# Performance work log

Measured on AMD Instinct MI355X. Metric: run time of the kernel, lower is better.

The kernel has to match this reference:

```python
import jax, jax.numpy as jnp
import numpy as np

TOPK = 2


def setup_inputs() -> dict:
    key = jax.random.key(0)
    k1, k2 = jax.random.split(key)
    B, N, D, E, C = 4, 2048, 2048, 8, 512
    token_inputs = jax.random.normal(k1, (B, N, D), dtype=jnp.float32)
    # bottleneck_in.weight.t() stacked over experts: [E, D, C]; scaled like a real init
    bottleneck_weights = jax.random.normal(k2, (E, D, C), dtype=jnp.float32) * 0.02
    return {
        "token_inputs": token_inputs,
        "bottleneck_weights": bottleneck_weights,
        "expert_capacity": 640,
    }


def _routing(router_probs, expert_capacity, topk):
    # router_probs: [B, N, E]
    B, N, E = router_probs.shape
    _, expert_indices = jax.lax.top_k(router_probs, topk)      # [B, N, topk]
    idx = jnp.transpose(expert_indices, (0, 2, 1)).reshape(B, topk * N)
    expert_mask = jax.nn.one_hot(idx, E, dtype=jnp.int32)       # [B, topk*N, E]
    token_priority = jnp.cumsum(expert_mask, axis=1) * expert_mask - 1
    token_priority = token_priority.reshape(B, topk, N, E)
    token_priority = jnp.transpose(token_priority, (0, 2, 1, 3))  # [B, N, topk, E]
    token_priority = jnp.max(token_priority, axis=2)              # [B, N, E]
    # one-hot over capacity; negative (-1) and >= capacity priorities map to all-zero rows
    cap_range = jnp.arange(expert_capacity, dtype=jnp.int32)
    dispatch = (token_priority[..., None] == cap_range).astype(jnp.float32)  # [B,N,E,C]
    combine = router_probs[..., None] * dispatch                            # [B,N,E,C]
    return dispatch, combine


def reference(token_inputs, bottleneck_weights, expert_capacity):
    # activation_cache: [B, N, E, Cb]
    activation_cache = jnp.einsum("bnd,edc->bnec", token_inputs, bottleneck_weights)
    router_logits = jnp.sqrt(jnp.sum(activation_cache * activation_cache, axis=-1))  # [B,N,E]
    router_probs = jax.nn.softmax(router_logits, axis=-1)
    dispatch, combine = _routing(router_probs, expert_capacity, TOPK)
    return jnp.stack([dispatch, combine], axis=0)  # [2, B, N, E, capacity]
```

## Files before the change

kernel.cpp:

```cpp
#include <hip/hip_runtime.h>
#include <math.h>

constexpr int Bb = 4, Nn = 2048, Dd = 2048, Ee = 8, Cbn = 512;
constexpr int Mm = Bb * Nn;

typedef _Float16 half8 __attribute__((ext_vector_type(8)));
typedef float floatx16 __attribute__((ext_vector_type(16)));

#define GLL16(g, l)                                                     \
  __builtin_amdgcn_global_load_lds(                                     \
      (const __attribute__((address_space(1))) void*)(g),               \
      (__attribute__((address_space(3))) void*)(l), 16, 0, 0)

#define MFMA_F16(a, b, c) __builtin_amdgcn_mfma_f32_32x32x16_f16(a, b, c, 0, 0, 0)


__global__ __launch_bounds__(256) void transpose_w(const float* __restrict__ W,
                                                   _Float16* __restrict__ WT) {
  const int kt = blockIdx.x;
  const int ct = blockIdx.y;
  const int e = blockIdx.z;
  __shared__ _Float16 thi[64][72];
  __shared__ _Float16 tlo[64][72];
  const int tx = threadIdx.x & 15, ty = threadIdx.x >> 4;
  const float* src = W + ((size_t)(e * 2048 + kt * 64)) * 512 + ct * 64;
#pragma unroll
  for (int p = 0; p < 4; ++p) {
    int kk = ty + p * 16;
    float4 v = *(const float4*)(src + (size_t)kk * 512 + tx * 4);
    _Float16 hh;
    hh = (_Float16)v.x; thi[tx * 4 + 0][kk] = hh; tlo[tx * 4 + 0][kk] = (_Float16)(v.x - (float)hh);
    hh = (_Float16)v.y; thi[tx * 4 + 1][kk] = hh; tlo[tx * 4 + 1][kk] = (_Float16)(v.y - (float)hh);
    hh = (_Float16)v.z; thi[tx * 4 + 2][kk] = hh; tlo[tx * 4 + 2][kk] = (_Float16)(v.z - (float)hh);
    hh = (_Float16)v.w; thi[tx * 4 + 3][kk] = hh; tlo[tx * 4 + 3][kk] = (_Float16)(v.w - (float)hh);
  }
  __syncthreads();
  const int nt = e * 4 + (ct >> 1);
#pragma unroll
  for (int p = 0; p < 2; ++p) {
    int unit = threadIdx.x + p * 256;
    int ch = unit >> 6;
    int cc = unit & 63;
    int kt16 = kt * 4 + (ch >> 1);
    int chunk = ch & 1;
    int row = (ct & 1) * 64 + cc;
    _Float16* dst = WT + ((size_t)(nt * 128 + kt16)) * 4096 + chunk * 1024 + row * 8;
    *(half8*)dst = *(const half8*)(&thi[cc][ch * 8]);
    *(half8*)(dst + 2048) = *(const half8*)(&tlo[cc][ch * 8]);
  }
}

__global__ __launch_bounds__(256) void split_x(const float* __restrict__ X,
                                               _Float16* __restrict__ XT) {
  const int mt = blockIdx.x;
  const int kb = blockIdx.y;
  const int tid = threadIdx.x;
#pragma unroll
  for (int p = 0; p < 2; ++p) {
    const int u = tid + p * 256;
    const int c4 = u & 3;
    const int row = u >> 2;
    const float* src = X + ((size_t)(mt * 128 + row)) * 2048 + kb * 32 + c4 * 8;
    float4 a = *(const float4*)src;
    float4 b = *(const float4*)(src + 4);
    float f[8] = {a.x, a.y, a.z, a.w, b.x, b.y, b.z, b.w};
    half8 hi, lo;
#pragma unroll
    for (int j = 0; j < 8; ++j) {
      _Float16 hh = (_Float16)f[j];
      hi[j] = hh;
      lo[j] = (_Float16)(f[j] - (float)hh);
    }
    const int kt16 = kb * 2 + (c4 >> 1);
    const int chunk = c4 & 1;
    _Float16* dst = XT + ((size_t)(mt * 128 + kt16)) * 4096 + chunk * 1024 + row * 8;
    *(half8*)dst = hi;
    *(half8*)(dst + 2048) = lo;
  }
}

__global__ __launch_bounds__(512) void gemm_mfma(const _Float16* __restrict__ XT,
                                                 const _Float16* __restrict__ WT,
                                                 float* __restrict__ partial) {
  const int bid = blockIdx.x;
  const int swz = (bid & 7) * 64 + (bid >> 3);
  const int bM = swz >> 4;
  const int bN = swz & 15;

  const int tid = threadIdx.x;
  const int w = tid >> 6, l = tid & 63;
  const int wm = w >> 2, wn = w & 3;
  const int h = l >> 5, l31 = l & 31;

  __shared__ __align__(16) char lds[131072];

  const char* XTb = (const char*)XT;
  const char* WTb = (const char*)WT;
  const char* srcA[2];
  const char* srcB[2];
  int ldsAo[2], ldsBo[2];
#pragma unroll
  for (int q = 0; q < 2; ++q) {
    const int i3 = q * 4 + (w >> 1);
    srcA[q] = XTb + ((size_t)((bM * 2 + (i3 >> 2)) * 128)) * 8192 +
              (i3 & 3) * 2048 + (w & 1) * 1024 + l * 16;
    srcB[q] = WTb + ((size_t)((bN * 2 + (i3 >> 2)) * 128)) * 8192 +
              (i3 & 3) * 2048 + (w & 1) * 1024 + l * 16;
    ldsAo[q] = q * 8192 + w * 1024;
    ldsBo[q] = 16384 + q * 8192 + w * 1024;
  }

  int aoff[4][2], boff[2][2];
#pragma unroll
  for (int mf = 0; mf < 4; ++mf)
#pragma unroll
    for (int hl = 0; hl < 2; ++hl)
      aoff[mf][hl] = wm * 8192 + hl * 4096 + h * 2048 + (mf * 32 + l31) * 16;
#pragma unroll
  for (int nf = 0; nf < 2; ++nf)
#pragma unroll
    for (int hl = 0; hl < 2; ++hl)
      boff[nf][hl] = 16384 + (wn >> 1) * 8192 + hl * 4096 + h * 2048 +
                     ((wn & 1) * 64 + nf * 32 + l31) * 16;

  floatx16 acc[4][2] = {};

  auto stage = [&](int t) {
    const size_t ko = (size_t)t * 8192;
    char* base = lds + (t & 3) * 32768;
#pragma unroll
    for (int q = 0; q < 2; ++q) {
      GLL16(srcA[q] + ko, base + ldsAo[q]);
      GLL16(srcB[q] + ko, base + ldsBo[q]);
    }
  };
  auto compute = [&](int t) {
    const char* Lb = lds + (t & 3) * 32768;
    half8 ah[4], al[4], bh[2], bl[2];
#pragma unroll
    for (int mf = 0; mf < 4; ++mf) {
      ah[mf] = *(const half8*)(Lb + aoff[mf][0]);
      al[mf] = *(const half8*)(Lb + aoff[mf][1]);
    }
#pragma unroll
    for (int nf = 0; nf < 2; ++nf) {
      bh[nf] = *(const half8*)(Lb + boff[nf][0]);
      bl[nf] = *(const half8*)(Lb + boff[nf][1]);
    }
    __builtin_amdgcn_s_setprio(1);
#pragma unroll
    for (int mf = 0; mf < 4; ++mf)
#pragma unroll
      for (int nf = 0; nf < 2; ++nf) {
        acc[mf][nf] = MFMA_F16(ah[mf], bh[nf], acc[mf][nf]);
        acc[mf][nf] = MFMA_F16(ah[mf], bl[nf], acc[mf][nf]);
        acc[mf][nf] = MFMA_F16(al[mf], bh[nf], acc[mf][nf]);
      }
    __builtin_amdgcn_s_setprio(0);
  };

  stage(0);
  stage(1);
  stage(2);
  asm volatile("s_waitcnt vmcnt(8)" ::: "memory");
  __builtin_amdgcn_s_barrier();

  for (int kt = 0; kt < 125; ++kt) {
    stage(kt + 3);
    compute(kt);
    asm volatile("s_waitcnt vmcnt(8)" ::: "memory");
    __builtin_amdgcn_s_barrier();
  }
  asm volatile("s_waitcnt vmcnt(0)" ::: "memory");
  __builtin_amdgcn_s_barrier();
  compute(125);
  compute(126);
  compute(127);

  const int slice = bN * 4 + wn;
  float out0 = 0.f, out1 = 0.f;
#pragma unroll
  for (int j = 0; j < 2; ++j) {
    float mv = 0.f;
#pragma unroll
    for (int ii = 0; ii < 2; ++ii) {
      const floatx16& c0 = acc[j * 2 + ii][0];
      const floatx16& c1 = acc[j * 2 + ii][1];
#pragma unroll
      for (int reg = 0; reg < 16; ++reg) {
        float v = c0[reg] * c0[reg] + c1[reg] * c1[reg];
#pragma unroll
        for (int m = 1; m <= 16; m <<= 1) v += __shfl_xor(v, m, 64);
        if (l31 == ii * 16 + reg) mv = v;
      }
    }
    if (j == 0) out0 = mv; else out1 = mv;
  }
  {
    const int reg = l & 15;
    const int ii = l31 >> 4;
    const int rowin = (reg & 3) + 8 * (reg >> 2) + 4 * h;
    const int tok = bM * 256 + wm * 128 + ii * 32 + rowin;
    partial[(size_t)tok * 64 + slice] = out0;
    partial[(size_t)(tok + 64) * 64 + slice] = out1;
  }
}

__global__ void route_kernel(const float* __restrict__ partial,
                             int* __restrict__ idx1, int* __restrict__ idx2,
                             float* __restrict__ p1, float* __restrict__ p2) {
  int t = blockIdx.x * blockDim.x + threadIdx.x;
  if (t >= Mm) return;
  float l[Ee];
  float mx = -1e30f;
#pragma unroll
  for (int e = 0; e < Ee; ++e) {
    float s = 0.f;
#pragma unroll
    for (int u = 0; u < 8; ++u) s += partial[(size_t)t * 64 + e * 8 + u];
    l[e] = sqrtf(s);
    mx = fmaxf(mx, l[e]);
  }
  float p[Ee];
  float s = 0.f;
#pragma unroll
  for (int e = 0; e < Ee; ++e) {
    p[e] = expf(l[e] - mx);
    s += p[e];
  }
  float inv = 1.f / s;
  int i1 = 0;
  float b1 = l[0];
#pragma unroll
  for (int e = 1; e < Ee; ++e)
    if (l[e] > b1) { b1 = l[e]; i1 = e; }
  int i2 = -1;
  float b2 = -1e30f;
#pragma unroll
  for (int e = 0; e < Ee; ++e)
    if (e != i1 && l[e] > b2) { b2 = l[e]; i2 = e; }
  idx1[t] = i1;
  idx2[t] = i2;
  p1[t] = p[i1] * inv;
  p2[t] = p[i2] * inv;
}

__global__ void scan_kernel(const int* __restrict__ idx1,
                            const int* __restrict__ idx2,
                            int* __restrict__ prios) {
  const int b = blockIdx.x;
  const int tid = threadIdx.x;
  __shared__ int cnts[256][8];
  int cnt[8] = {0, 0, 0, 0, 0, 0, 0, 0};
  int eloc[16];
  const int base_p = tid * 16;
#pragma unroll
  for (int i = 0; i < 16; ++i) {
    int p = base_p + i;
    int k = p >> 11;
    int n = p & (Nn - 1);
    int e = (k == 0 ? idx1 : idx2)[b * Nn + n];
    eloc[i] = e;
    cnt[e]++;
  }
#pragma unroll
  for (int e = 0; e < 8; ++e) cnts[tid][e] = cnt[e];
  __syncthreads();
  if (tid < 8) {
    int run = 0;
    for (int i = 0; i < 256; ++i) {
      int v = cnts[i][tid];
      cnts[i][tid] = run;
      run += v;
    }
  }
  __syncthreads();
  int base[8];
#pragma unroll
  for (int e = 0; e < 8; ++e) base[e] = cnts[tid][e];
#pragma unroll
  for (int i = 0; i < 16; ++i) {
    int e = eloc[i];
    prios[b * 2 * Nn + base_p + i] = base[e]++;
  }
}

__global__ __launch_bounds__(256) void zscatter_kernel(const int* __restrict__ idx1,
                                                       const int* __restrict__ idx2,
                                                       const float* __restrict__ p1,
                                                       const float* __restrict__ p2,
                                                       const int* __restrict__ prios,
                                                       float* __restrict__ out, int cap) {
  const int t = blockIdx.x;
  const int ec = Ee * cap;
  float4* o1 = (float4*)(out + (size_t)t * ec);
  float4* o2 = (float4*)(out + (size_t)(Mm + t) * ec);
  const float4 z = make_float4(0.f, 0.f, 0.f, 0.f);
  const int n4 = ec / 4;
  for (int i = threadIdx.x; i < n4; i += 256) {
    o1[i] = z;
    o2[i] = z;
  }
  __syncthreads();
  if (threadIdx.x == 0) {
    const int b = t >> 11;
    const int n = t & (Nn - 1);
    int e = idx1[t];
    int p = prios[b * 2 * Nn + n];
    if (p < cap) {
      out[(size_t)t * ec + e * cap + p] = 1.f;
      out[(size_t)(Mm + t) * ec + e * cap + p] = p1[t];
    }
    e = idx2[t];
    p = prios[b * 2 * Nn + Nn + n];
    if (p < cap) {
      out[(size_t)t * ec + e * cap + p] = 1.f;
      out[(size_t)(Mm + t) * ec + e * cap + p] = p2[t];
    }
  }
}

extern "C" void kernel_launch(void* const* d_in, const int* in_sizes, int n_in,
                              void* d_out, int out_size, void* d_ws, size_t ws_size,
                              hipStream_t stream) {
  const float* X = (const float*)d_in[0];
  const float* W = (const float*)d_in[1];
  float* out = (float*)d_out;
  const int cap = out_size / (2 * Bb * Nn * Ee);

  char* ws = (char*)d_ws;
  _Float16* WT = (_Float16*)ws;
  float* partial = (float*)(ws + 33554432ull);
  int* idx1 = (int*)(ws + 35651584ull);
  int* idx2 = idx1 + Mm;
  float* p1 = (float*)(idx2 + Mm);
  float* p2 = p1 + Mm;
  int* prios = (int*)(p2 + Mm);

  _Float16* XT = (_Float16*)d_out;

  transpose_w<<<dim3(32, 8, 8), 256, 0, stream>>>(W, WT);
  split_x<<<dim3(64, 64), 256, 0, stream>>>(X, XT);
  gemm_mfma<<<512, 512, 0, stream>>>(XT, WT, partial);
  route_kernel<<<Mm / 256, 256, 0, stream>>>(partial, idx1, idx2, p1, p2);
  scan_kernel<<<Bb, 256, 0, stream>>>(idx1, idx2, prios);
  zscatter_kernel<<<Mm, 256, 0, stream>>>(idx1, idx2, p1, p2, prios, out, cap);
}
```

Measured before the change: 757.5 us.

## Merge prep kernels, double K-step GEMM with 2-stage buffer, fuse route and scan

Combines the weight transpose and X split into one launch, and merges routing with the priority scan into a single per-batch kernel that uses a parallel wave-level prefix scan instead of a serial 8-thread loop. The GEMM now loads 32 K-elements per stage into two 64KB LDS buffers instead of 16 per stage into four, halving the number of barriers but reducing prefetch depth to one stage with a full vmcnt(0) wait. This cuts launch count and sync overhead at the risk of exposing more global-load latency in the GEMM. The route_scan kernel runs only 4 blocks, so the routing math that previously ran across 32 blocks now sits on 4 CUs.

```diff
diff --git a/kernel.cpp b/kernel.cpp
--- a/kernel.cpp
+++ b/kernel.cpp
@@ -15,67 +15,70 @@
 #define MFMA_F16(a, b, c) __builtin_amdgcn_mfma_f32_32x32x16_f16(a, b, c, 0, 0, 0)
 
 
-__global__ __launch_bounds__(256) void transpose_w(const float* __restrict__ W,
-                                                   _Float16* __restrict__ WT) {
-  const int kt = blockIdx.x;
-  const int ct = blockIdx.y;
-  const int e = blockIdx.z;
+__global__ __launch_bounds__(256) void prep_kernel(const float* __restrict__ W,
+                                                   _Float16* __restrict__ WT,
+                                                   const float* __restrict__ X,
+                                                   _Float16* __restrict__ XT) {
   __shared__ _Float16 thi[64][72];
   __shared__ _Float16 tlo[64][72];
-  const int tx = threadIdx.x & 15, ty = threadIdx.x >> 4;
-  const float* src = W + ((size_t)(e * 2048 + kt * 64)) * 512 + ct * 64;
-#pragma unroll
-  for (int p = 0; p < 4; ++p) {
-    int kk = ty + p * 16;
-    float4 v = *(const float4*)(src + (size_t)kk * 512 + tx * 4);
-    _Float16 hh;
-    hh = (_Float16)v.x; thi[tx * 4 + 0][kk] = hh; tlo[tx * 4 + 0][kk] = (_Float16)(v.x - (float)hh);
-    hh = (_Float16)v.y; thi[tx * 4 + 1][kk] = hh; tlo[tx * 4 + 1][kk] = (_Float16)(v.y - (float)hh);
-    hh = (_Float16)v.z; thi[tx * 4 + 2][kk] = hh; tlo[tx * 4 + 2][kk] = (_Float16)(v.z - (float)hh);
-    hh = (_Float16)v.w; thi[tx * 4 + 3][kk] = hh; tlo[tx * 4 + 3][kk] = (_Float16)(v.w - (float)hh);
-  }
-  __syncthreads();
-  const int nt = e * 4 + (ct >> 1);
-#pragma unroll
-  for (int p = 0; p < 2; ++p) {
-    int unit = threadIdx.x + p * 256;
-    int ch = unit >> 6;
-    int cc = unit & 63;
-    int kt16 = kt * 4 + (ch >> 1);
-    int chunk = ch & 1;
-    int row = (ct & 1) * 64 + cc;
-    _Float16* dst = WT + ((size_t)(nt * 128 + kt16)) * 4096 + chunk * 1024 + row * 8;
-    *(half8*)dst = *(const half8*)(&thi[cc][ch * 8]);
-    *(half8*)(dst + 2048) = *(const half8*)(&tlo[cc][ch * 8]);
-  }
-}
-
-__global__ __launch_bounds__(256) void split_x(const float* __restrict__ X,
-                                               _Float16* __restrict__ XT) {
-  const int mt = blockIdx.x;
-  const int kb = blockIdx.y;
-  const int tid = threadIdx.x;
-#pragma unroll
-  for (int p = 0; p < 2; ++p) {
-    const int u = tid + p * 256;
-    const int c4 = u & 3;
-    const int row = u >> 2;
-    const float* src = X + ((size_t)(mt * 128 + row)) * 2048 + kb * 32 + c4 * 8;
-    float4 a = *(const float4*)src;
-    float4 b = *(const float4*)(src + 4);
-    float f[8] = {a.x, a.y, a.z, a.w, b.x, b.y, b.z, b.w};
-    half8 hi, lo;
-#pragma unroll
-    for (int j = 0; j < 8; ++j) {
-      _Float16 hh = (_Float16)f[j];
-      hi[j] = hh;
-      lo[j] = (_Float16)(f[j] - (float)hh);
-    }
-    const int kt16 = kb * 2 + (c4 >> 1);
-    const int chunk = c4 & 1;
-    _Float16* dst = XT + ((size_t)(mt * 128 + kt16)) * 4096 + chunk * 1024 + row * 8;
-    *(half8*)dst = hi;
-    *(half8*)(dst + 2048) = lo;
+  const int bid = blockIdx.x;
+  if (bid < 2048) {
+    const int kt = bid & 31;
+    const int ct = (bid >> 5) & 7;
+    const int e = bid >> 8;
+    const int tx = threadIdx.x & 15, ty = threadIdx.x >> 4;
+    const float* src = W + ((size_t)(e * 2048 + kt * 64)) * 512 + ct * 64;
+#pragma unroll
+    for (int p = 0; p < 4; ++p) {
+      int kk = ty + p * 16;
+      float4 v = *(const float4*)(src + (size_t)kk * 512 + tx * 4);
+      _Float16 hh;
+      hh = (_Float16)v.x; thi[tx * 4 + 0][kk] = hh; tlo[tx * 4 + 0][kk] = (_Float16)(v.x - (float)hh);
+      hh = (_Float16)v.y; thi[tx * 4 + 1][kk] = hh; tlo[tx * 4 + 1][kk] = (_Float16)(v.y - (float)hh);
+      hh = (_Float16)v.z; thi[tx * 4 + 2][kk] = hh; tlo[tx * 4 + 2][kk] = (_Float16)(v.z - (float)hh);
+      hh = (_Float16)v.w; thi[tx * 4 + 3][kk] = hh; tlo[tx * 4 + 3][kk] = (_Float16)(v.w - (float)hh);
+    }
+    __syncthreads();
+    const int nt = e * 4 + (ct >> 1);
+#pragma unroll
+    for (int p = 0; p < 2; ++p) {
+      int unit = threadIdx.x + p * 256;
+      int ch = unit >> 6;
+      int cc = unit & 63;
+      int kt16 = kt * 4 + (ch >> 1);
+      int chunk = ch & 1;
+      int row = (ct & 1) * 64 + cc;
+      _Float16* dst = WT + ((size_t)(nt * 128 + kt16)) * 4096 + chunk * 1024 + row * 8;
+      *(half8*)dst = *(const half8*)(&thi[cc][ch * 8]);
+      *(half8*)(dst + 2048) = *(const half8*)(&tlo[cc][ch * 8]);
+    }
+  } else {
+    const int id = bid - 2048;
+    const int mt = id & 63;
+    const int kb = id >> 6;
+    const int tid = threadIdx.x;
+#pragma unroll
+    for (int p = 0; p < 2; ++p) {
+      const int u = tid + p * 256;
+      const int c4 = u & 3;
+      const int row = u >> 2;
+      const float* src = X + ((size_t)(mt * 128 + row)) * 2048 + kb * 32 + c4 * 8;
+      float4 a = *(const float4*)src;
+      float4 b = *(const float4*)(src + 4);
+      float f[8] = {a.x, a.y, a.z, a.w, b.x, b.y, b.z, b.w};
+      half8 hi, lo;
+#pragma unroll
+      for (int j = 0; j < 8; ++j) {
+        _Float16 hh = (_Float16)f[j];
+        hi[j] = hh;
+        lo[j] = (_Float16)(f[j] - (float)hh);
+      }
+      const int kt16 = kb * 2 + (c4 >> 1);
+      const int chunk = c4 & 1;
+      _Float16* dst = XT + ((size_t)(mt * 128 + kt16)) * 4096 + chunk * 1024 + row * 8;
+      *(half8*)dst = hi;
+      *(half8*)(dst + 2048) = lo;
+    }
   }
 }
 
@@ -96,86 +99,86 @@
 
   const char* XTb = (const char*)XT;
   const char* WTb = (const char*)WT;
-  const char* srcA[2];
-  const char* srcB[2];
-  int ldsAo[2], ldsBo[2];
-#pragma unroll
-  for (int q = 0; q < 2; ++q) {
-    const int i3 = q * 4 + (w >> 1);
-    srcA[q] = XTb + ((size_t)((bM * 2 + (i3 >> 2)) * 128)) * 8192 +
-              (i3 & 3) * 2048 + (w & 1) * 1024 + l * 16;
-    srcB[q] = WTb + ((size_t)((bN * 2 + (i3 >> 2)) * 128)) * 8192 +
-              (i3 & 3) * 2048 + (w & 1) * 1024 + l * 16;
-    ldsAo[q] = q * 8192 + w * 1024;
-    ldsBo[q] = 16384 + q * 8192 + w * 1024;
-  }
-
-  int aoff[4][2], boff[2][2];
-#pragma unroll
-  for (int mf = 0; mf < 4; ++mf)
-#pragma unroll
-    for (int hl = 0; hl < 2; ++hl)
-      aoff[mf][hl] = wm * 8192 + hl * 4096 + h * 2048 + (mf * 32 + l31) * 16;
-#pragma unroll
-  for (int nf = 0; nf < 2; ++nf)
-#pragma unroll
-    for (int hl = 0; hl < 2; ++hl)
-      boff[nf][hl] = 16384 + (wn >> 1) * 8192 + hl * 4096 + h * 2048 +
-                     ((wn & 1) * 64 + nf * 32 + l31) * 16;
+  const char* srcA[4];
+  const char* srcB[4];
+  int ldsAo[4], ldsBo[4];
+#pragma unroll
+  for (int q = 0; q < 4; ++q) {
+    const int c = q * 8 + w;
+    const int ht = c >> 4, k16 = (c >> 3) & 1, u = c & 7;
+    srcA[q] = XTb + (size_t)(bM * 2 + ht) * 1048576 + k16 * 8192 + u * 1024 + l * 16;
+    srcB[q] = WTb + (size_t)(bN * 2 + ht) * 1048576 + k16 * 8192 + u * 1024 + l * 16;
+    ldsAo[q] = c * 1024;
+    ldsBo[q] = 32768 + c * 1024;
+  }
+
+  int aoff[2][4][2], boff[2][2][2];
+#pragma unroll
+  for (int k16 = 0; k16 < 2; ++k16) {
+#pragma unroll
+    for (int mf = 0; mf < 4; ++mf)
+#pragma unroll
+      for (int hl = 0; hl < 2; ++hl)
+        aoff[k16][mf][hl] = wm * 16384 + k16 * 8192 + hl * 4096 + h * 2048 +
+                            (mf * 32 + l31) * 16;
+#pragma unroll
+    for (int nf = 0; nf < 2; ++nf)
+#pragma unroll
+      for (int hl = 0; hl < 2; ++hl)
+        boff[k16][nf][hl] = 32768 + (wn >> 1) * 16384 + k16 * 8192 + hl * 4096 + h * 2048 +
+                            ((wn & 1) * 64 + nf * 32 + l31) * 16;
+  }
 
   floatx16 acc[4][2] = {};
 
   auto stage = [&](int t) {
-    const size_t ko = (size_t)t * 8192;
-    char* base = lds + (t & 3) * 32768;
-#pragma unroll
-    for (int q = 0; q < 2; ++q) {
+    const size_t ko = (size_t)t * 16384;
+    char* base = lds + (t & 1) * 65536;
+#pragma unroll
+    for (int q = 0; q < 4; ++q) {
       GLL16(srcA[q] + ko, base + ldsAo[q]);
       GLL16(srcB[q] + ko, base + ldsBo[q]);
     }
   };
   auto compute = [&](int t) {
-    const char* Lb = lds + (t & 3) * 32768;
-    half8 ah[4], al[4], bh[2], bl[2];
-#pragma unroll
-    for (int mf = 0; mf < 4; ++mf) {
-      ah[mf] = *(const half8*)(Lb + aoff[mf][0]);
-      al[mf] = *(const half8*)(Lb + aoff[mf][1]);
-    }
-#pragma unroll
-    for (int nf = 0; nf < 2; ++nf) {
-      bh[nf] = *(const half8*)(Lb + boff[nf][0]);
-      bl[nf] = *(const half8*)(Lb + boff[nf][1]);
-    }
-    __builtin_amdgcn_s_setprio(1);
-#pragma unroll
-    for (int mf = 0; mf < 4; ++mf)
+    const char* Lb = lds + (t & 1) * 65536;
+#pragma unroll
+    for (int k16 = 0; k16 < 2; ++k16) {
+      half8 ah[4], al[4], bh[2], bl[2];
+#pragma unroll
+      for (int mf = 0; mf < 4; ++mf) {
+        ah[mf] = *(const half8*)(Lb + aoff[k16][mf][0]);
+        al[mf] = *(const half8*)(Lb + aoff[k16][mf][1]);
+      }
 #pragma unroll
       for (int nf = 0; nf < 2; ++nf) {
-        acc[mf][nf] = MFMA_F16(ah[mf], bh[nf], acc[mf][nf]);
-        acc[mf][nf] = MFMA_F16(ah[mf], bl[nf], acc[mf][nf]);
-        acc[mf][nf] = MFMA_F16(al[mf], bh[nf], acc[mf][nf]);
+        bh[nf] = *(const half8*)(Lb + boff[k16][nf][0]);
+        bl[nf] = *(const half8*)(Lb + boff[k16][nf][1]);
       }
-    __builtin_amdgcn_s_setprio(0);
+      __builtin_amdgcn_s_setprio(1);
+#pragma unroll
+      for (int mf = 0; mf < 4; ++mf)
+#pragma unroll
+        for (int nf = 0; nf < 2; ++nf) {
+          acc[mf][nf] = MFMA_F16(ah[mf], bh[nf], acc[mf][nf]);
+          acc[mf][nf] = MFMA_F16(ah[mf], bl[nf], acc[mf][nf]);
+          acc[mf][nf] = MFMA_F16(al[mf], bh[nf], acc[mf][nf]);
+        }
+      __builtin_amdgcn_s_setprio(0);
+    }
   };
 
   stage(0);
-  stage(1);
-  stage(2);
-  asm volatile("s_waitcnt vmcnt(8)" ::: "memory");
-  __builtin_amdgcn_s_barrier();
-
-  for (int kt = 0; kt < 125; ++kt) {
-    stage(kt + 3);
-    compute(kt);
-    asm volatile("s_waitcnt vmcnt(8)" ::: "memory");
-    __builtin_amdgcn_s_barrier();
-  }
   asm volatile("s_waitcnt vmcnt(0)" ::: "memory");
   __builtin_amdgcn_s_barrier();
-  compute(125);
-  compute(126);
-  compute(127);
+
+  for (int kt = 0; kt < 63; ++kt) {
+    stage(kt + 1);
+    compute(kt);
+    asm volatile("s_waitcnt vmcnt(0)" ::: "memory");
+    __builtin_amdgcn_s_barrier();
+  }
+  compute(63);
 
   const int slice = bN * 4 + wn;
   float out0 = 0.f, out1 = 0.f;
@@ -206,82 +209,102 @@
   }
 }
 
-__global__ void route_kernel(const float* __restrict__ partial,
-                             int* __restrict__ idx1, int* __restrict__ idx2,
-                             float* __restrict__ p1, float* __restrict__ p2) {
-  int t = blockIdx.x * blockDim.x + threadIdx.x;
-  if (t >= Mm) return;
-  float l[Ee];
-  float mx = -1e30f;
-#pragma unroll
-  for (int e = 0; e < Ee; ++e) {
-    float s = 0.f;
-#pragma unroll
-    for (int u = 0; u < 8; ++u) s += partial[(size_t)t * 64 + e * 8 + u];
-    l[e] = sqrtf(s);
-    mx = fmaxf(mx, l[e]);
-  }
-  float p[Ee];
-  float s = 0.f;
-#pragma unroll
-  for (int e = 0; e < Ee; ++e) {
-    p[e] = expf(l[e] - mx);
-    s += p[e];
-  }
-  float inv = 1.f / s;
-  int i1 = 0;
-  float b1 = l[0];
-#pragma unroll
-  for (int e = 1; e < Ee; ++e)
-    if (l[e] > b1) { b1 = l[e]; i1 = e; }
-  int i2 = -1;
-  float b2 = -1e30f;
-#pragma unroll
-  for (int e = 0; e < Ee; ++e)
-    if (e != i1 && l[e] > b2) { b2 = l[e]; i2 = e; }
-  idx1[t] = i1;
-  idx2[t] = i2;
-  p1[t] = p[i1] * inv;
-  p2[t] = p[i2] * inv;
-}
-
-__global__ void scan_kernel(const int* __restrict__ idx1,
-                            const int* __restrict__ idx2,
-                            int* __restrict__ prios) {
+__global__ __launch_bounds__(1024) void route_scan(const float* __restrict__ partial,
+                                                   int* __restrict__ idx1,
+                                                   int* __restrict__ idx2,
+                                                   float* __restrict__ p1,
+                                                   float* __restrict__ p2,
+                                                   int* __restrict__ prios) {
   const int b = blockIdx.x;
   const int tid = threadIdx.x;
-  __shared__ int cnts[256][8];
-  int cnt[8] = {0, 0, 0, 0, 0, 0, 0, 0};
-  int eloc[16];
-  const int base_p = tid * 16;
-#pragma unroll
-  for (int i = 0; i < 16; ++i) {
-    int p = base_p + i;
-    int k = p >> 11;
-    int n = p & (Nn - 1);
-    int e = (k == 0 ? idx1 : idx2)[b * Nn + n];
+  __shared__ unsigned char e1s[2048], e2s[2048];
+  __shared__ int cnts[1024][9];
+
+#pragma unroll
+  for (int r = 0; r < 2; ++r) {
+    const int n = tid * 2 + r;
+    const int t = b * 2048 + n;
+    const float4* pr = (const float4*)(partial + (size_t)t * 64);
+    float l[Ee];
+    float mx = -1e30f;
+#pragma unroll
+    for (int e = 0; e < Ee; ++e) {
+      float4 s0 = pr[e * 2], s1 = pr[e * 2 + 1];
+      float s = s0.x + s0.y + s0.z + s0.w + s1.x + s1.y + s1.z + s1.w;
+      l[e] = sqrtf(s);
+      mx = fmaxf(mx, l[e]);
+    }
+    float p[Ee];
+    float s = 0.f;
+#pragma unroll
+    for (int e = 0; e < Ee; ++e) {
+      p[e] = expf(l[e] - mx);
+      s += p[e];
+    }
+    float inv = 1.f / s;
+    int i1 = 0;
+    float b1 = l[0];
+#pragma unroll
+    for (int e = 1; e < Ee; ++e)
+      if (l[e] > b1) { b1 = l[e]; i1 = e; }
+    int i2 = -1;
+    float b2 = -1e30f;
+#pragma unroll
+    for (int e = 0; e < Ee; ++e)
+      if (e != i1 && l[e] > b2) { b2 = l[e]; i2 = e; }
+    idx1[t] = i1;
+    idx2[t] = i2;
+    p1[t] = p[i1] * inv;
+    p2[t] = p[i2] * inv;
+    e1s[n] = (unsigned char)i1;
+    e2s[n] = (unsigned char)i2;
+  }
+  __syncthreads();
+
+  int cnt[Ee] = {0, 0, 0, 0, 0, 0, 0, 0};
+  int eloc[4];
+#pragma unroll
+  for (int i = 0; i < 4; ++i) {
+    const int p = tid * 4 + i;
+    const int e = (p >> 11) ? (int)e2s[p & 2047] : (int)e1s[p & 2047];
     eloc[i] = e;
     cnt[e]++;
   }
 #pragma unroll
-  for (int e = 0; e < 8; ++e) cnts[tid][e] = cnt[e];
+  for (int e = 0; e < Ee; ++e) cnts[tid][e] = cnt[e];
   __syncthreads();
-  if (tid < 8) {
-    int run = 0;
-    for (int i = 0; i < 256; ++i) {
-      int v = cnts[i][tid];
-      cnts[i][tid] = run;
-      run += v;
+
+  const int wv = tid >> 6, ln = tid & 63;
+  if (wv < 8) {
+    int loc[16];
+    int s = 0;
+#pragma unroll
+    for (int i = 0; i < 16; ++i) {
+      loc[i] = cnts[ln * 16 + i][wv];
+      s += loc[i];
+    }
+    int x = s;
+#pragma unroll
+    for (int off = 1; off < 64; off <<= 1) {
+      int y = __shfl_up(x, off, 64);
+      if (ln >= off) x += y;
+    }
+    int run = x - s;
+#pragma unroll
+    for (int i = 0; i < 16; ++i) {
+      int tmp = loc[i];
+      cnts[ln * 16 + i][wv] = run;
+      run += tmp;
     }
   }
   __syncthreads();
-  int base[8];
-#pragma unroll
-  for (int e = 0; e < 8; ++e) base[e] = cnts[tid][e];
-#pragma unroll
-  for (int i = 0; i < 16; ++i) {
-    int e = eloc[i];
-    prios[b * 2 * Nn + base_p + i] = base[e]++;
+
+  int base[Ee];
+#pragma unroll
+  for (int e = 0; e < Ee; ++e) base[e] = cnts[tid][e];
+#pragma unroll
+  for (int i = 0; i < 4; ++i) {
+    prios[b * 4096 + tid * 4 + i] = base[eloc[i]]++;
   }
 }
 
@@ -339,10 +362,8 @@
 
   _Float16* XT = (_Float16*)d_out;
 
-  transpose_w<<<dim3(32, 8, 8), 256, 0, stream>>>(W, WT);
-  split_x<<<dim3(64, 64), 256, 0, stream>>>(X, XT);
+  prep_kernel<<<6144, 256, 0, stream>>>(W, WT, X, XT);
   gemm_mfma<<<512, 512, 0, stream>>>(XT, WT, partial);
-  route_kernel<<<Mm / 256, 256, 0, stream>>>(partial, idx1, idx2, p1, p2);
-  scan_kernel<<<Bb, 256, 0, stream>>>(idx1, idx2, prios);
+  route_scan<<<Bb, 1024, 0, stream>>>(partial, idx1, idx2, p1, p2, prios);
   zscatter_kernel<<<Mm, 256, 0, stream>>>(idx1, idx2, p1, p2, prios, out, cap);
 }
```

New measurement: 763.3 us. Within noise of the previous version (+0.8%).
